# Optimization experiments

Measured on AMD Instinct MI355X. Metric: run time of the kernel, lower is better.

Reference implementation:

```python
import jax, jax.numpy as jnp
import numpy as np

HIDDEN = 1024
N_HEADS = 16
HEAD_DIM = HIDDEN // N_HEADS  # 64


def setup_inputs() -> dict:
    key = jax.random.key(0)
    ks = jax.random.split(key, 5)
    B, S = 4, 4096
    x = jax.random.normal(ks[0], (B, S, HIDDEN), dtype=jnp.float32)
    scale = 1.0 / np.sqrt(HIDDEN)
    wq = jax.random.normal(ks[1], (HIDDEN, HIDDEN), dtype=jnp.float32) * scale
    wk = jax.random.normal(ks[2], (HIDDEN, HIDDEN), dtype=jnp.float32) * scale
    wv = jax.random.normal(ks[3], (HIDDEN, HIDDEN), dtype=jnp.float32) * scale
    wo = jax.random.normal(ks[4], (HIDDEN, HIDDEN), dtype=jnp.float32) * scale
    return {"x": x, "wq": wq, "wk": wk, "wv": wv, "wo": wo}


def reference(x, wq, wk, wv, wo):
    # Weights stored as (out, in) like torch nn.Linear; y = x @ W^T
    B, S, H = x.shape
    q = (x @ wq.T).reshape(B, S, N_HEADS, HEAD_DIM)
    k = (x @ wk.T).reshape(B, S, N_HEADS, HEAD_DIM)
    v = (x @ wv.T).reshape(B, S, N_HEADS, HEAD_DIM)
    # Faithful to original: no transpose to (B,H,S,D) -> scores are over HEADS
    # attn: (B, S, H_heads, H_heads)
    attn = jnp.einsum("bshd,bsgd->bshg", q, k) / np.sqrt(HEAD_DIM)
    attn = jax.nn.softmax(attn, axis=-1)
    out = jnp.einsum("bshg,bsgd->bshd", attn, v).reshape(B, S, H)
    return out @ wo.T
```

## Files before the change

### kernel.cpp

```cpp
#include <hip/hip_runtime.h>
#include <hip/hip_bf16.h>


typedef __bf16 bf16;
typedef __attribute__((ext_vector_type(8))) __bf16 bf16x8;
typedef __attribute__((ext_vector_type(4))) float floatx4;

#define HIDDEN 1024
#define BM 128
#define BN 128
#define BK 32

#define FENCE() asm volatile("" ::: "memory")
#define BAR()                                                                  \
    do {                                                                       \
        FENCE();                                                               \
        __builtin_amdgcn_s_barrier();                                          \
        FENCE();                                                               \
    } while (0)
#define VMCNT(N) asm volatile("s_waitcnt vmcnt(" #N ")" ::: "memory")

__device__ __forceinline__ void async_load16(const bf16* g, bf16* lds) {
    __builtin_amdgcn_global_load_lds(
        (const __attribute__((address_space(1))) void*)g,
        (__attribute__((address_space(3))) void*)lds, 16, 0, 0);
}

__device__ __forceinline__ bf16x8 load8(const bf16* p) {
    return *(const bf16x8*)p;
}
__device__ __forceinline__ bf16x8 load8(const float* p) {
    floatx4 lo = *(const floatx4*)p;
    floatx4 hi = *(const floatx4*)(p + 4);
    bf16x8 r;
#pragma unroll
    for (int i = 0; i < 4; ++i) { r[i] = (bf16)lo[i]; r[i + 4] = (bf16)hi[i]; }
    return r;
}

__global__ __launch_bounds__(256) void cvt_all(
    const float* __restrict__ x,
    const float* __restrict__ wq, const float* __restrict__ wk,
    const float* __restrict__ wv, const float* __restrict__ wo,
    bf16* __restrict__ xb, bf16* __restrict__ wpk, int mh8)
{
    const int per = (HIDDEN * HIDDEN) / 8;
    int i = blockIdx.x * 256 + threadIdx.x;
    if (i < mh8) {
        *(bf16x8*)&xb[(size_t)i * 8] = load8(&x[(size_t)i * 8]);
    } else {
        int j = i - mh8;
        int wsel = j / per;
        int off  = (j - wsel * per) * 8;
        const float* s = wsel == 0 ? wq : wsel == 1 ? wk : wsel == 2 ? wv : wo;
        *(bf16x8*)&wpk[(size_t)j * 8] = load8(&s[off]);
    }
}


template <int S>
__device__ __forceinline__ void stage_half(const bf16* __restrict__ gbase,
                                           int ld, int kt, bf16* lhalf,
                                           int h, int tid) {
#pragma unroll
    for (int j = 0; j < 2; ++j) {
        const int ci = j * 512 + tid;
        const int rr = ci >> 3;
        const int cs = (ci & 7) ^ (rr & 7);
        const int gr = h * S + (rr & (S - 1)) + (rr >> (S == 64 ? 6 : 5)) * (2 * S);
        async_load16(&gbase[(size_t)gr * ld + kt + cs * 8], &lhalf[ci * 8]);
    }
}

__device__ __forceinline__ void ld_a4(const bf16* h, int wm, int col, int quad,
                                      int cx, bf16x8* a) {
#pragma unroll
    for (int i = 0; i < 4; ++i) {
        const int rr = i * 16 + col + (wm << 6);
#pragma unroll
        for (int kk = 0; kk < 2; ++kk)
            a[i * 2 + kk] =
                *(const bf16x8*)&h[rr * 64 + (((kk << 2) + quad) ^ cx) * 8];
    }
}
__device__ __forceinline__ void ld_b2(const bf16* h, int wn, int col, int quad,
                                      int cx, bf16x8* b) {
#pragma unroll
    for (int j = 0; j < 2; ++j) {
        const int rr = j * 16 + col + (wn << 5);
#pragma unroll
        for (int kk = 0; kk < 2; ++kk)
            b[j * 2 + kk] =
                *(const bf16x8*)&h[rr * 64 + (((kk << 2) + quad) ^ cx) * 8];
    }
}

template <int H, int G>
__device__ __forceinline__ void mmq(floatx4 (&acc)[8][4], const bf16x8 (&a)[8],
                                    const bf16x8 (&bb)[4]) {
    __builtin_amdgcn_s_setprio(1);
#pragma unroll
    for (int i = 0; i < 4; ++i)
#pragma unroll
        for (int j = 0; j < 2; ++j)
#pragma unroll
            for (int kk = 0; kk < 2; ++kk)
                acc[H * 4 + i][G * 2 + j] =
                    __builtin_amdgcn_mfma_f32_16x16x32_bf16(
                        a[i * 2 + kk], bb[j * 2 + kk],
                        acc[H * 4 + i][G * 2 + j], 0, 0, 0);
    __builtin_amdgcn_s_setprio(0);
}

template <typename TC>
__global__ __launch_bounds__(512, 2) void gemm8p(
    const bf16* __restrict__ A, const bf16* __restrict__ W,
    TC* __restrict__ C, int K, int lda, int ldc)
{
    __shared__ __align__(16) bf16 sA[2][2][128 * 64];
    __shared__ __align__(16) bf16 sB[2][2][128 * 64];

    const int tid  = threadIdx.x;
    const int lane = tid & 63;
    const int w    = tid >> 6;
    const int wm   = w >> 2;
    const int wn   = w & 3;
    const int m0   = blockIdx.x * 256;
    const int n0   = blockIdx.y * 256;
    const int col  = lane & 15;
    const int quad = lane >> 4;
    const int cx   = col & 7;

    const bf16* Ab = A + (size_t)m0 * lda;
    const bf16* Wb = W + (size_t)n0 * K;

    floatx4 acc[8][4] = {};
    bf16x8 a[8], b0[4], b1[4];

    const int T = K / 64;

    stage_half<64>(Ab, lda, 0, sA[0][0], 0, tid);
    stage_half<32>(Wb, K,   0, sB[0][0], 0, tid);
    stage_half<32>(Wb, K,   0, sB[0][1], 1, tid);
    stage_half<64>(Ab, lda, 0, sA[0][1], 1, tid);
    if (T > 1) {
        stage_half<64>(Ab, lda, 64, sA[1][0], 0, tid);
        stage_half<32>(Wb, K,   64, sB[1][0], 0, tid);
        stage_half<32>(Wb, K,   64, sB[1][1], 1, tid);
        VMCNT(6);
    } else {
        VMCNT(0);
    }
    BAR();

    for (int t = 0; t < T; ++t) {
        const int b   = t & 1;
        const int kt1 = (t + 1) * 64;
        const int kt2 = (t + 2) * 64;

        ld_a4(sA[b][0], wm, col, quad, cx, a);
        ld_b2(sB[b][0], wn, col, quad, cx, b0);
        if (t + 1 < T) stage_half<64>(Ab, lda, kt1, sA[b ^ 1][1], 1, tid);
        VMCNT(8);
        BAR();
        mmq<0, 0>(acc, a, b0);
        BAR();

        ld_b2(sB[b][1], wn, col, quad, cx, b1);
        if (t + 2 < T) stage_half<64>(Ab, lda, kt2, sA[b][0], 0, tid);
        VMCNT(8);
        BAR();
        mmq<0, 1>(acc, a, b1);
        BAR();

        ld_a4(sA[b][1], wm, col, quad, cx, a);
        if (t + 2 < T) stage_half<32>(Wb, K, kt2, sB[b][0], 0, tid);
        VMCNT(8);
        BAR();
        mmq<1, 1>(acc, a, b1);
        BAR();

        if (t + 2 < T) stage_half<32>(Wb, K, kt2, sB[b][1], 1, tid);
        VMCNT(8);
        BAR();
        mmq<1, 0>(acc, a, b0);
        BAR();
    }

#pragma unroll
    for (int mi = 0; mi < 8; ++mi) {
#pragma unroll
        for (int r = 0; r < 4; ++r) {
            const int row = m0 + wm * 128 + mi * 16 + quad * 4 + r;
#pragma unroll
            for (int ni = 0; ni < 4; ++ni) {
                const int cc = n0 + wn * 64 + ni * 16 + col;
                C[(size_t)row * ldc + cc] = (TC)acc[mi][ni][r];
            }
        }
    }
}

template <typename TA, typename TB, typename TC>
__global__ __launch_bounds__(256, 2) void gemm_bt(
    const TA* __restrict__ A, const TB* __restrict__ W,
    TC* __restrict__ C, int M, int N, int K)
{
    __shared__ __align__(16) bf16 sA[BM * BK];
    __shared__ __align__(16) bf16 sB[BN * BK];

    const int tid  = threadIdx.x;
    const int lane = tid & 63;
    const int w    = tid >> 6;
    const int wm   = w >> 1;
    const int wn   = w & 1;
    const int m0   = blockIdx.x * BM;
    const int n0   = blockIdx.y * BN;
    const int col  = lane & 15;
    const int quad = lane >> 4;

    floatx4 acc[4][4] = {};

    for (int kt = 0; kt < K; kt += BK) {
        bf16x8 ga[2], gb[2];
#pragma unroll
        for (int i = 0; i < 2; ++i) {
            const int c   = i * 256 + tid;
            const int row = c >> 2;
            const int kc  = c & 3;
            ga[i] = load8(&A[(size_t)(m0 + row) * K + kt + kc * 8]);
            gb[i] = load8(&W[(size_t)(n0 + row) * K + kt + kc * 8]);
        }
        __syncthreads();
#pragma unroll
        for (int i = 0; i < 2; ++i) {
            const int c = i * 256 + tid;
            *(bf16x8*)&sA[c * 8] = ga[i];
            *(bf16x8*)&sB[c * 8] = gb[i];
        }
        __syncthreads();

        bf16x8 af[4], bfr[4];
#pragma unroll
        for (int mi = 0; mi < 4; ++mi)
            af[mi] = *(const bf16x8*)&sA[(wm * 64 + mi * 16 + col) * BK + quad * 8];
#pragma unroll
        for (int ni = 0; ni < 4; ++ni)
            bfr[ni] = *(const bf16x8*)&sB[(wn * 64 + ni * 16 + col) * BK + quad * 8];

#pragma unroll
        for (int mi = 0; mi < 4; ++mi)
#pragma unroll
            for (int ni = 0; ni < 4; ++ni)
                acc[mi][ni] = __builtin_amdgcn_mfma_f32_16x16x32_bf16(
                    af[mi], bfr[ni], acc[mi][ni], 0, 0, 0);
    }

#pragma unroll
    for (int mi = 0; mi < 4; ++mi) {
#pragma unroll
        for (int r = 0; r < 4; ++r) {
            const int row = m0 + wm * 64 + mi * 16 + quad * 4 + r;
#pragma unroll
            for (int ni = 0; ni < 4; ++ni) {
                const int cc = n0 + wn * 64 + ni * 16 + col;
                C[(size_t)row * N + cc] = (TC)acc[mi][ni][r];
            }
        }
    }
}

__global__ __launch_bounds__(256) void attn_heads(
    bf16* base, size_t koff, size_t voff, int stride, bf16* ob)
{
    __shared__ __align__(16) bf16 sP[4][16 * 40];
    __shared__ __align__(16) bf16 sVt[4][64 * 40];

    const int tid   = threadIdx.x;
    const int lane  = tid & 63;
    const int w     = tid >> 6;
    const int token = blockIdx.x * 4 + w;
    const int col   = lane & 15;
    const int quad  = lane >> 4;

    bf16* qt = base + (size_t)token * stride;
    const bf16* kt = qt + koff;
    const bf16* vt = qt + voff;
    bf16* ot = ob + (size_t)token * HIDDEN;

    const bf16x8 z = {};
    *(bf16x8*)&sVt[w][lane * 40 + 16] = z;
    *(bf16x8*)&sVt[w][lane * 40 + 24] = z;
    if (lane < 16) {
        *(bf16x8*)&sP[w][lane * 40 + 16] = z;
        *(bf16x8*)&sP[w][lane * 40 + 24] = z;
    }

    bf16x8 qa0 = *(const bf16x8*)&qt[col * 64 + quad * 8];
    bf16x8 qa1 = *(const bf16x8*)&qt[col * 64 + 32 + quad * 8];
    bf16x8 kb0 = *(const bf16x8*)&kt[col * 64 + quad * 8];
    bf16x8 kb1 = *(const bf16x8*)&kt[col * 64 + 32 + quad * 8];
    floatx4 s = {};
    s = __builtin_amdgcn_mfma_f32_16x16x32_bf16(qa0, kb0, s, 0, 0, 0);
    s = __builtin_amdgcn_mfma_f32_16x16x32_bf16(qa1, kb1, s, 0, 0, 0);

    bf16x8 vc0, vc1;
#pragma unroll
    for (int j = 0; j < 8; ++j)  vc0[j] = vt[j * 64 + lane];
#pragma unroll
    for (int j = 0; j < 8; ++j)  vc1[j] = vt[(j + 8) * 64 + lane];
    *(bf16x8*)&sVt[w][lane * 40]     = vc0;
    *(bf16x8*)&sVt[w][lane * 40 + 8] = vc1;

#pragma unroll
    for (int r = 0; r < 4; ++r) {
        float x = s[r] * 0.125f;
        float m = x;
#pragma unroll
        for (int off = 1; off < 16; off <<= 1)
            m = fmaxf(m, __shfl_xor(m, off));
        float e = __expf(x - m);
        float su = e;
#pragma unroll
        for (int off = 1; off < 16; off <<= 1)
            su += __shfl_xor(su, off);
        sP[w][(quad * 4 + r) * 40 + col] = (bf16)(e / su);
    }

    bf16x8 pa = *(const bf16x8*)&sP[w][col * 40 + quad * 8];
#pragma unroll
    for (int dt = 0; dt < 4; ++dt) {
        bf16x8 vb = *(const bf16x8*)&sVt[w][(dt * 16 + col) * 40 + quad * 8];
        floatx4 o4 = {};
        o4 = __builtin_amdgcn_mfma_f32_16x16x32_bf16(pa, vb, o4, 0, 0, 0);
#pragma unroll
        for (int r = 0; r < 4; ++r)
            ot[(quad * 4 + r) * 64 + dt * 16 + col] = (bf16)o4[r];
    }
}

extern "C" void kernel_launch(void* const* d_in, const int* in_sizes, int n_in,
                              void* d_out, int out_size, void* d_ws, size_t ws_size,
                              hipStream_t stream) {
    const float* x  = (const float*)d_in[0];
    const float* wq = (const float*)d_in[1];
    const float* wk = (const float*)d_in[2];
    const float* wv = (const float*)d_in[3];
    const float* wo = (const float*)d_in[4];
    float* out = (float*)d_out;

    const int M = in_sizes[0] / HIDDEN;
    const size_t MH = (size_t)M * HIDDEN;
    const size_t WH = (size_t)HIDDEN * HIDDEN;

    const size_t need = (MH + 4 * WH + (size_t)M * 3 * HIDDEN) * sizeof(bf16);

    if (ws_size >= need && (M % 256) == 0) {
        bf16* xb  = (bf16*)d_ws;
        bf16* wpk = xb + MH;
        bf16* qkv = wpk + 4 * WH;

        const int mh8 = (int)(MH / 8);
        const int nchunks = mh8 + (int)(4 * WH / 8);
        cvt_all<<<dim3(nchunks / 256), 256, 0, stream>>>(x, wq, wk, wv, wo,
                                                         xb, wpk, mh8);

        gemm8p<bf16><<<dim3(M / 256, 3 * HIDDEN / 256), 512, 0, stream>>>(
            xb, wpk, qkv, HIDDEN, HIDDEN, 3 * HIDDEN);

        attn_heads<<<dim3(M / 4), 256, 0, stream>>>(qkv, 1024, 2048,
                                                    3 * HIDDEN, xb);

        gemm8p<float><<<dim3(M / 256, HIDDEN / 256), 512, 0, stream>>>(
            xb, wpk + 3 * WH, out, HIDDEN, HIDDEN, HIDDEN);
    } else {
        bf16* qb = (bf16*)d_ws;
        bf16* kb = qb + MH;
        bf16* vb = kb + MH;
        dim3 grid(M / BM, HIDDEN / BN), block(256);
        gemm_bt<float, float, bf16><<<grid, block, 0, stream>>>(x, wq, qb, M, HIDDEN, HIDDEN);
        gemm_bt<float, float, bf16><<<grid, block, 0, stream>>>(x, wk, kb, M, HIDDEN, HIDDEN);
        gemm_bt<float, float, bf16><<<grid, block, 0, stream>>>(x, wv, vb, M, HIDDEN, HIDDEN);
        attn_heads<<<dim3(M / 4), block, 0, stream>>>(qb, MH, 2 * MH, HIDDEN, qb);
        gemm_bt<bf16, float, float><<<grid, block, 0, stream>>>(qb, wo, out, M, HIDDEN, HIDDEN);
    }
}
```

Before: 288.5 us.

## Rework GEMM prefetch schedule, add XCD block remap, simplify head attention

Result: no change. 291.4 us (+1.0%).

```diff
diff --git a/kernel.cpp b/kernel.cpp
--- a/kernel.cpp
+++ b/kernel.cpp
@@ -11,14 +11,13 @@
 #define BN 128
 #define BK 32
 
-#define FENCE() asm volatile("" ::: "memory")
-#define BAR()                                                                  \
+#define VMCNT(N) asm volatile("s_waitcnt vmcnt(" #N ")" ::: "memory")
+#define LGKM0()                                                                \
     do {                                                                       \
-        FENCE();                                                               \
-        __builtin_amdgcn_s_barrier();                                          \
-        FENCE();                                                               \
+        asm volatile("s_waitcnt lgkmcnt(0)" ::: "memory");                     \
+        __builtin_amdgcn_sched_barrier(0);                                     \
     } while (0)
-#define VMCNT(N) asm volatile("s_waitcnt vmcnt(" #N ")" ::: "memory")
+#define SBAR() __builtin_amdgcn_s_barrier()
 
 __device__ __forceinline__ void async_load16(const bf16* g, bf16* lds) {
     __builtin_amdgcn_global_load_lds(
@@ -125,11 +124,19 @@
     const int w    = tid >> 6;
     const int wm   = w >> 2;
     const int wn   = w & 3;
-    const int m0   = blockIdx.x * 256;
-    const int n0   = blockIdx.y * 256;
     const int col  = lane & 15;
     const int quad = lane >> 4;
     const int cx   = col & 7;
+
+    const int gx = gridDim.x, gy = gridDim.y;
+    const int nwg = gx * gy;
+    int lin = blockIdx.y * gx + blockIdx.x;
+    if ((nwg & 7) == 0) {
+        const int cpx = nwg >> 3;
+        lin = (lin & 7) * cpx + (lin >> 3);
+    }
+    const int m0 = (lin / gy) * 256;
+    const int n0 = (lin % gy) * 256;
 
     const bf16* Ab = A + (size_t)m0 * lda;
     const bf16* Wb = W + (size_t)n0 * K;
@@ -151,40 +158,45 @@
     } else {
         VMCNT(0);
     }
-    BAR();
+    SBAR();
 
     for (int t = 0; t < T; ++t) {
-        const int b   = t & 1;
-        const int kt1 = (t + 1) * 64;
-        const int kt2 = (t + 2) * 64;
+        const int b = t & 1;
 
         ld_a4(sA[b][0], wm, col, quad, cx, a);
         ld_b2(sB[b][0], wn, col, quad, cx, b0);
-        if (t + 1 < T) stage_half<64>(Ab, lda, kt1, sA[b ^ 1][1], 1, tid);
-        VMCNT(8);
-        BAR();
+        if (t + 1 < T) stage_half<64>(Ab, lda, (t + 1) * 64, sA[b ^ 1][1], 1, tid);
+        SBAR();
+        LGKM0();
         mmq<0, 0>(acc, a, b0);
-        BAR();
+        SBAR();
 
         ld_b2(sB[b][1], wn, col, quad, cx, b1);
-        if (t + 2 < T) stage_half<64>(Ab, lda, kt2, sA[b][0], 0, tid);
-        VMCNT(8);
-        BAR();
+        SBAR();
+        LGKM0();
         mmq<0, 1>(acc, a, b1);
-        BAR();
+        SBAR();
 
         ld_a4(sA[b][1], wm, col, quad, cx, a);
-        if (t + 2 < T) stage_half<32>(Wb, K, kt2, sB[b][0], 0, tid);
-        VMCNT(8);
-        BAR();
+        if (t + 2 < T) {
+            stage_half<64>(Ab, lda, (t + 2) * 64, sA[b][0], 0, tid);
+            stage_half<32>(Wb, K,   (t + 2) * 64, sB[b][0], 0, tid);
+        }
+        SBAR();
+        LGKM0();
         mmq<1, 1>(acc, a, b1);
-        BAR();
-
-        if (t + 2 < T) stage_half<32>(Wb, K, kt2, sB[b][1], 1, tid);
-        VMCNT(8);
-        BAR();
+        SBAR();
+
+        if (t + 2 < T) {
+            stage_half<32>(Wb, K, (t + 2) * 64, sB[b][1], 1, tid);
+            VMCNT(6);
+        } else {
+            VMCNT(0);
+        }
+        SBAR();
+        LGKM0();
         mmq<1, 0>(acc, a, b0);
-        BAR();
+        SBAR();
     }
 
 #pragma unroll
@@ -274,7 +286,6 @@
     bf16* base, size_t koff, size_t voff, int stride, bf16* ob)
 {
     __shared__ __align__(16) bf16 sP[4][16 * 40];
-    __shared__ __align__(16) bf16 sVt[4][64 * 40];
 
     const int tid   = threadIdx.x;
     const int lane  = tid & 63;
@@ -288,12 +299,13 @@
     const bf16* vt = qt + voff;
     bf16* ot = ob + (size_t)token * HIDDEN;
 
-    const bf16x8 z = {};
-    *(bf16x8*)&sVt[w][lane * 40 + 16] = z;
-    *(bf16x8*)&sVt[w][lane * 40 + 24] = z;
-    if (lane < 16) {
-        *(bf16x8*)&sP[w][lane * 40 + 16] = z;
-        *(bf16x8*)&sP[w][lane * 40 + 24] = z;
+    bf16x8 vb[4] = {};
+    if (quad < 2) {
+#pragma unroll
+        for (int dt = 0; dt < 4; ++dt)
+#pragma unroll
+            for (int j = 0; j < 8; ++j)
+                vb[dt][j] = vt[(quad * 8 + j) * 64 + dt * 16 + col];
     }
 
     bf16x8 qa0 = *(const bf16x8*)&qt[col * 64 + quad * 8];
@@ -304,22 +316,9 @@
     s = __builtin_amdgcn_mfma_f32_16x16x32_bf16(qa0, kb0, s, 0, 0, 0);
     s = __builtin_amdgcn_mfma_f32_16x16x32_bf16(qa1, kb1, s, 0, 0, 0);
 
-    bf16x8 vc0, vc1;
-#pragma unroll
-    for (int j = 0; j < 8; ++j)  vc0[j] = vt[j * 64 + lane];
-#pragma unroll
-    for (int j = 0; j < 8; ++j)  vc1[j] = vt[(j + 8) * 64 + lane];
-    *(bf16x8*)&sVt[w][lane * 40]     = vc0;
-    *(bf16x8*)&sVt[w][lane * 40 + 8] = vc1;
-
 #pragma unroll
     for (int r = 0; r < 4; ++r) {
-        float x = s[r] * 0.125f;
-        float m = x;
-#pragma unroll
-        for (int off = 1; off < 16; off <<= 1)
-            m = fmaxf(m, __shfl_xor(m, off));
-        float e = __expf(x - m);
+        float e = __expf(s[r] * 0.125f);
         float su = e;
 #pragma unroll
         for (int off = 1; off < 16; off <<= 1)
@@ -327,12 +326,12 @@
         sP[w][(quad * 4 + r) * 40 + col] = (bf16)(e / su);
     }
 
-    bf16x8 pa = *(const bf16x8*)&sP[w][col * 40 + quad * 8];
+    bf16x8 pa = {};
+    if (quad < 2) pa = *(const bf16x8*)&sP[w][col * 40 + quad * 8];
 #pragma unroll
     for (int dt = 0; dt < 4; ++dt) {
-        bf16x8 vb = *(const bf16x8*)&sVt[w][(dt * 16 + col) * 40 + quad * 8];
         floatx4 o4 = {};
-        o4 = __builtin_amdgcn_mfma_f32_16x16x32_bf16(pa, vb, o4, 0, 0, 0);
+        o4 = __builtin_amdgcn_mfma_f32_16x16x32_bf16(pa, vb[dt], o4, 0, 0, 0);
 #pragma unroll
         for (int r = 0; r < 4; ++r)
             ot[(quad * 4 + r) * 64 + dt * 16 + col] = (bf16)o4[r];
```
